# Kernel tuning notes

Hardware: AMD Instinct MI355X
Metric: run time of the kernel (lower is better)

The kernel has to match this reference:

```python
import jax, jax.numpy as jnp
import numpy as np

IN_DIM = 512
HID = 256
SAMPLE = 8
TAU = 0.5
LAMBDA = 1.0
NUM_MLP = 3


def l2norm(x, axis=-1, eps=1e-12):
    n = jnp.sqrt(jnp.sum(x * x, axis=axis, keepdims=True))
    return x / jnp.maximum(n, eps)


def graphconv(adj, x, W, b):
    # GraphConv: aggregate then linear transform
    return adj @ (x @ W) + b


def mlp(x, Ws, bs):
    h = x
    for i in range(len(Ws) - 1):
        h = jax.nn.relu(h @ Ws[i] + bs[i])
    return h @ Ws[-1] + bs[-1]


def setup_inputs() -> dict:
    key = jax.random.key(0)
    ks = jax.random.split(key, 24)
    N = 16384
    # sparse-ish row-normalized adjacency surrogate (dense storage)
    a1 = jax.random.uniform(ks[0], (N, N), jnp.float32)
    a1 = (a1 > 0.999).astype(jnp.float32)
    adj1 = a1 / jnp.maximum(a1.sum(1, keepdims=True), 1.0)
    a2 = jax.random.uniform(ks[1], (N, N), jnp.float32)
    a2 = (a2 > 0.999).astype(jnp.float32)
    adj2 = a2 / jnp.maximum(a2.sum(1, keepdims=True), 1.0)
    x1 = jax.random.normal(ks[2], (N, IN_DIM), jnp.float32)
    x2 = jax.random.normal(ks[3], (N, IN_DIM), jnp.float32)
    neighbor_idx = jax.random.randint(ks[4], (N, SAMPLE), 0, N)
    neg_idx = jax.random.randint(ks[5], (N, SAMPLE), 0, N)

    def lin(k, fi, fo):
        k1, k2 = jax.random.split(k)
        s = 1.0 / np.sqrt(fi)
        return (jax.random.uniform(k1, (fi, fo), jnp.float32, -s, s),
                jax.random.uniform(k2, (fo,), jnp.float32, -s, s))

    W1, b1 = lin(ks[6], IN_DIM, HID)
    W2, b2 = lin(ks[7], HID, HID)
    tW1, tb1 = lin(ks[8], IN_DIM, HID)
    tW2, tb2 = lin(ks[9], HID, HID)
    projW, projB, semW, semB = [], [], [], []
    for i in range(NUM_MLP):
        w, b = lin(ks[10 + i], HID, HID)
        projW.append(w); projB.append(b)
        w, b = lin(ks[14 + i], HID, HID)
        semW.append(w); semB.append(b)
    return dict(adj1=adj1, adj2=adj2, x1=x1, x2=x2,
                neighbor_idx=neighbor_idx, neg_idx=neg_idx,
                W1=W1, b1=b1, W2=W2, b2=b2,
                tW1=tW1, tb1=tb1, tW2=tW2, tb2=tb2,
                projW0=projW[0], projB0=projB[0], projW1=projW[1], projB1=projB[1], projW2=projW[2], projB2=projB[2],
                semW0=semW[0], semB0=semB[0], semW1=semW[1], semB1=semB[1], semW2=semW[2], semB2=semB[2])


def contrastive_loss(projected_emd, v_emd, samp_u, samp_neg_v):
    # projected_emd, v_emd: [N,1,D]; samp_u, samp_neg_v: [N,S,D]
    pos = jnp.exp(jnp.einsum('nod,nsd->ns', projected_emd, samp_u) / TAU)  # [N,S]
    neg_sum = jnp.sum(jnp.exp(jnp.einsum('nod,nsd->ns', v_emd, samp_neg_v) / TAU), axis=1)  # [N]
    neg_score = jnp.sum(jnp.log(pos + neg_sum[:, None]), axis=1)  # [N]
    pos_score = jnp.sum(jnp.log(pos), axis=1)
    total = jnp.sum(LAMBDA * neg_score - pos_score)
    return total / samp_u.shape[0] / samp_u.shape[1]


def semi_loss(z1, z2):
    z1n = l2norm(z1); z2n = l2norm(z2)
    refl = jnp.exp((z1n @ z1n.T) / TAU)      # [N,N]
    between = jnp.exp((z1n @ z2n.T) / TAU)   # [N,N]
    return -jnp.log(jnp.diagonal(between) / (refl.sum(1) + between.sum(1) - jnp.diagonal(refl)))


def reference(adj1, adj2, x1, x2, neighbor_idx, neg_idx,
              W1, b1, W2, b2, tW1, tb1, tW2, tb2,
              projW0, projB0, projW1, projB1, projW2, projB2,
              semW0, semB0, semW1, semB1, semW2, semB2):
    pW = [projW0, projW1, projW2]; pB = [projB0, projB1, projB2]
    sW = [semW0, semW1, semW2]; sB = [semB0, semB1, semB2]
    h1 = graphconv(adj1, x1, W1, b1)
    h2 = graphconv(adj1, x2, W1, b1)
    h3 = graphconv(adj2, graphconv(adj2, x1, W1, b1), W2, b2)  # v_emd
    u_emd = l2norm(graphconv(adj2, graphconv(adj2, x1, tW1, tb1), tW2, tb2))
    projected = l2norm(mlp(h3, pW, pB))
    h1_proj = l2norm(mlp(h1, sW, sB))
    h2_proj = l2norm(mlp(h2, sW, sB))

    v_norm = l2norm(h3)
    samp_u = u_emd[neighbor_idx]          # [N,S,D]
    samp_neg_v = v_norm[neg_idx]          # [N,S,D]
    gacl = contrastive_loss(projected[:, None, :], v_norm[:, None, :], samp_u, samp_neg_v)

    l1 = semi_loss(h1_proj, h2_proj)
    l2 = semi_loss(h2_proj, h1_proj)
    sem = jnp.mean((l1 + l2) * 0.5)

    total = gacl + 0.6 * sem
    return total, gacl, sem, h3
```

## Files before the change

### kernel.cpp

```cpp
#include <hip/hip_runtime.h>
#include <hip/hip_bf16.h>

#define NN   16384
#define IND  512
#define HID  256
#define SAMP 8
#define CAP  64

typedef __bf16 bf16;
typedef __bf16 bf16x4 __attribute__((ext_vector_type(4)));
typedef __bf16 bf16x8 __attribute__((ext_vector_type(8)));
typedef float  f32x4  __attribute__((ext_vector_type(4)));

#define LOG2E_2 2.8853900817779268f

#define GLOAD_LDS16(gptr, lptr) \
  __builtin_amdgcn_global_load_lds((const __attribute__((address_space(1))) void*)(gptr), \
                                   (__attribute__((address_space(3))) void*)(lptr), 16, 0, 0)

__global__ void cvt_x(const float* __restrict__ a, bf16* __restrict__ oa,
                      const float* __restrict__ b, bf16* __restrict__ ob) {
  const float* src = blockIdx.y ? b : a;
  bf16* dst = blockIdx.y ? ob : oa;
  int stride = gridDim.x * blockDim.x;
  for (int i = blockIdx.x * blockDim.x + threadIdx.x; i < (NN * IND) / 4; i += stride) {
    float4 v = ((const float4*)src)[i];
    bf16x4 o = {(bf16)v.x, (bf16)v.y, (bf16)v.z, (bf16)v.w};
    *(bf16x4*)(dst + (size_t)i * 4) = o;
  }
}

struct WtArgs {
  const float* src[10];
  bf16* dst[10];
  int K[10];
};

__global__ void cvt_weights(WtArgs a) {
  int w = blockIdx.y;
  int K = a.K[w];
  int total = K * HID;
  const float* s = a.src[w];
  bf16* d = a.dst[w];
  for (int i = blockIdx.x * blockDim.x + threadIdx.x; i < total; i += gridDim.x * blockDim.x) {
    int k = i >> 8, n = i & 255;
    d[n * K + k] = (bf16)s[i];
  }
}

__global__ void scan_adj(const float* __restrict__ adjA, const float* __restrict__ adjB,
                         int* __restrict__ colsA, int* __restrict__ cntA,
                         int* __restrict__ colsB, int* __restrict__ cntB) {
  const float* adj = blockIdx.y ? adjB : adjA;
  int* cols = blockIdx.y ? colsB : colsA;
  int* cnt = blockIdx.y ? cntB : cntA;
  int r = blockIdx.x;
  __shared__ int c;
  if (threadIdx.x == 0) c = 0;
  __syncthreads();
  const float4* row = (const float4*)(adj + (size_t)r * NN);
  int* rc = cols + (size_t)r * CAP;
  #pragma unroll 4
  for (int i = threadIdx.x; i < NN / 4; i += 256) {
    float4 v = row[i];
    if (v.x != 0.f || v.y != 0.f || v.z != 0.f || v.w != 0.f) {
      if (v.x != 0.f) { int p = atomicAdd(&c, 1); if (p < CAP) rc[p] = 4 * i; }
      if (v.y != 0.f) { int p = atomicAdd(&c, 1); if (p < CAP) rc[p] = 4 * i + 1; }
      if (v.z != 0.f) { int p = atomicAdd(&c, 1); if (p < CAP) rc[p] = 4 * i + 2; }
      if (v.w != 0.f) { int p = atomicAdd(&c, 1); if (p < CAP) rc[p] = 4 * i + 3; }
    }
  }
  __syncthreads();
  if (threadIdx.x == 0) cnt[r] = (c < CAP) ? c : CAP;
}

struct SpmmB {
  const int* cols[4]; const int* cnt[4]; const bf16* X[4]; const float* bias[4];
  float* outF[4];
  bf16* outB[4];
  float* outNF[4];
};
__global__ void spmm_b(SpmmB s) {
  int j = blockIdx.y;
  int wid = threadIdx.x >> 6, lane = threadIdx.x & 63;
  int r = blockIdx.x * 4 + wid;
  int c = s.cnt[j][r];
  float val = 1.0f / (float)(c > 0 ? c : 1);
  const int* rc = s.cols[j] + (size_t)r * CAP;
  const bf16* X = s.X[j];
  float ax = 0.f, ay = 0.f, az = 0.f, aw = 0.f;
  for (int t = 0; t < c; ++t) {
    int col = rc[t];
    bf16x4 v = *(const bf16x4*)(X + (size_t)col * HID + lane * 4);
    ax += (float)v[0]; ay += (float)v[1]; az += (float)v[2]; aw += (float)v[3];
  }
  float4 b4 = ((const float4*)s.bias[j])[lane];
  ax = ax * val + b4.x; ay = ay * val + b4.y; az = az * val + b4.z; aw = aw * val + b4.w;
  if (s.outF[j]) {
    float* o = s.outF[j] + (size_t)r * HID + lane * 4;
    o[0] = ax; o[1] = ay; o[2] = az; o[3] = aw;
  }
  if (s.outB[j]) {
    bf16x4 ob = {(bf16)ax, (bf16)ay, (bf16)az, (bf16)aw};
    *(bf16x4*)(s.outB[j] + (size_t)r * HID + lane * 4) = ob;
  }
  if (s.outNF[j]) {
    float ss = ax * ax + ay * ay + az * az + aw * aw;
    #pragma unroll
    for (int off = 1; off < 64; off <<= 1) ss += __shfl_xor(ss, off);
    float inv = 1.0f / fmaxf(sqrtf(ss), 1e-12f);
    float4 o = {ax * inv, ay * inv, az * inv, aw * inv};
    ((float4*)(s.outNF[j] + (size_t)r * HID))[lane] = o;
  }
}

struct GemmB {
  const bf16* A[3]; const bf16* Bt[3]; const float* bias[3];
  float* Cf[3]; bf16* Cb[3];
};
__global__ __launch_bounds__(256) void gemm_b(GemmB g, int K, int relu) {
  __shared__ bf16 As[128][64];
  __shared__ bf16 Bs[128][64];
  int j = blockIdx.z;
  const bf16* A = g.A[j];
  const bf16* Bt = g.Bt[j];
  int m0 = blockIdx.x * 128, n0 = blockIdx.y * 128;
  int tid = threadIdx.x, wid = tid >> 6, lane = tid & 63;
  int wm = wid >> 1, wn = wid & 1, q = lane >> 4, li = lane & 15;
  int r8 = lane >> 3, cc8 = lane & 7;
  int csw = cc8 ^ r8;
  f32x4 acc[4][4] = {};
  for (int k0 = 0; k0 < K; k0 += 64) {
    if (k0) __syncthreads();
    const bf16* gA = A + (size_t)(m0 + wid * 32 + r8) * K + k0 + csw * 8;
    const bf16* gB = Bt + (size_t)(n0 + wid * 32 + r8) * K + k0 + csw * 8;
    #pragma unroll
    for (int jj = 0; jj < 4; ++jj) {
      GLOAD_LDS16(gA + (size_t)jj * 8 * K, &As[wid * 32 + jj * 8][0]);
      GLOAD_LDS16(gB + (size_t)jj * 8 * K, &Bs[wid * 32 + jj * 8][0]);
    }
    __syncthreads();
    #pragma unroll
    for (int kk = 0; kk < 64; kk += 32) {
      int ca = (((q + (kk >> 3)) ^ (li & 7)) << 3);
      bf16x8 af[4], bfr[4];
      #pragma unroll
      for (int im = 0; im < 4; ++im) af[im] = *(const bf16x8*)(&As[wm * 64 + im * 16 + li][ca]);
      #pragma unroll
      for (int in = 0; in < 4; ++in) bfr[in] = *(const bf16x8*)(&Bs[wn * 64 + in * 16 + li][ca]);
      #pragma unroll
      for (int im = 0; im < 4; ++im)
        #pragma unroll
        for (int in = 0; in < 4; ++in)
          acc[im][in] = __builtin_amdgcn_mfma_f32_16x16x32_bf16(af[im], bfr[in], acc[im][in], 0, 0, 0);
    }
  }
  float* Cf = g.Cf[j];
  bf16* Cb = g.Cb[j];
  const float* bias = g.bias[j];
  #pragma unroll
  for (int im = 0; im < 4; ++im) {
    int grow0 = m0 + wm * 64 + im * 16 + q * 4;
    #pragma unroll
    for (int in = 0; in < 4; ++in) {
      int gcol = n0 + wn * 64 + in * 16 + li;
      float bv = bias ? bias[gcol] : 0.f;
      #pragma unroll
      for (int reg = 0; reg < 4; ++reg) {
        float v = acc[im][in][reg] + bv;
        if (relu) v = fmaxf(v, 0.f);
        size_t idx = (size_t)(grow0 + reg) * HID + gcol;
        if (Cf) Cf[idx] = v;
        if (Cb) Cb[idx] = (bf16)v;
      }
    }
  }
}

__global__ __launch_bounds__(256, 1) void flash_sem5(
    const bf16* __restrict__ P, const bf16* __restrict__ Q,
    float* __restrict__ Ra, float* __restrict__ Rb,
    float* __restrict__ Cr, float* __restrict__ Cc) {
  __shared__ bf16 As[2][128 * 256];
  int z = blockIdx.z;
  const bf16 *X, *Y;
  float* out;
  if (z == 0)      { X = P; Y = P; out = Ra; }
  else if (z == 1) { X = Q; Y = Q; out = Rb; }
  else if (z == 2) { X = P; Y = Q; out = Cc; }
  else             { X = Q; Y = P; out = Cr; }
  int tid = threadIdx.x, wid = tid >> 6, lane = tid & 63;
  int q = lane >> 4, li = lane & 15;
  int cbase = blockIdx.x * 512 + wid * 128;
  bf16x8 bfrag[8][8];
  #pragma unroll
  for (int in = 0; in < 8; ++in) {
    const bf16* Yr = Y + (size_t)(cbase + in * 16 + li) * HID + q * 8;
    #pragma unroll
    for (int kk = 0; kk < 8; ++kk)
      bfrag[in][kk] = *(const bf16x8*)(Yr + kk * 32);
  }
  float cs[8] = {};
  int i0 = blockIdx.y * (NN / 2);
  int l5 = lane >> 5, cp = lane & 31;
  auto stage = [&](int chunk, int b) {
    const bf16* src = X + (size_t)(i0 + chunk * 128) * HID;
    #pragma unroll
    for (int n = 0; n < 16; ++n) {
      int idx = wid * 16 + n;
      int r = idx * 2 + l5;
      int csrc = cp ^ (r & 31);
      GLOAD_LDS16(src + (size_t)r * HID + csrc * 8, &As[b][idx * 512]);
    }
  };
  stage(0, 0);
  __syncthreads();
  for (int c = 0; c < 64; ++c) {
    int b = c & 1;
    if (c + 1 < 64) stage(c + 1, b ^ 1);
    const bf16* buf = &As[b][0];
    #pragma unroll
    for (int ii = 0; ii < 8; ++ii) {
      bf16x8 af[8];
      #pragma unroll
      for (int kk = 0; kk < 8; ++kk) {
        int r = ii * 16 + li;
        int c16 = (kk * 4 + q) ^ (r & 31);
        af[kk] = *(const bf16x8*)(buf + r * 256 + c16 * 8);
      }
      f32x4 acc[8] = {};
      #pragma unroll
      for (int kk = 0; kk < 8; ++kk)
        #pragma unroll
        for (int in = 0; in < 8; ++in)
          acc[in] = __builtin_amdgcn_mfma_f32_16x16x32_bf16(af[kk], bfrag[in][kk], acc[in], 0, 0, 0);
      #pragma unroll
      for (int in = 0; in < 8; ++in)
        #pragma unroll
        for (int reg = 0; reg < 4; ++reg)
          cs[in] += exp2f(acc[in][reg] * LOG2E_2);
    }
    __syncthreads();
  }
  #pragma unroll
  for (int in = 0; in < 8; ++in) {
    float v = cs[in];
    v += __shfl_xor(v, 16);
    v += __shfl_xor(v, 32);
    if (q == 0) atomicAdd(&out[cbase + in * 16 + li], v);
  }
}

struct NormB { const float* X[3]; float* outF[3]; bf16* outB[3]; };
__global__ void l2norm_b(NormB n) {
  int j = blockIdx.y;
  int wid = threadIdx.x >> 6, lane = threadIdx.x & 63;
  int r = blockIdx.x * 4 + wid;
  float4 a = ((const float4*)(n.X[j] + (size_t)r * HID))[lane];
  float s = a.x * a.x + a.y * a.y + a.z * a.z + a.w * a.w;
  #pragma unroll
  for (int off = 1; off < 64; off <<= 1) s += __shfl_xor(s, off);
  float inv = 1.0f / fmaxf(sqrtf(s), 1e-12f);
  a.x *= inv; a.y *= inv; a.z *= inv; a.w *= inv;
  if (n.outF[j]) ((float4*)(n.outF[j] + (size_t)r * HID))[lane] = a;
  if (n.outB[j]) {
    bf16x4 b = {(bf16)a.x, (bf16)a.y, (bf16)a.z, (bf16)a.w};
    *(bf16x4*)(n.outB[j] + (size_t)r * HID + lane * 4) = b;
  }
}

__global__ void tail_k(const float* __restrict__ proj, const float* __restrict__ vn,
                       const float* __restrict__ ue, const int* __restrict__ nbr,
                       const int* __restrict__ neg,
                       const float* __restrict__ P, const float* __restrict__ Q2,
                       const float* __restrict__ Ra, const float* __restrict__ Rb,
                       const float* __restrict__ Cr, const float* __restrict__ Cc,
                       float* __restrict__ sums) {
  int wid = threadIdx.x >> 6, lane = threadIdx.x & 63;
  int n = blockIdx.x * 4 + wid;
  if (blockIdx.y == 0) {
    float4 p = ((const float4*)(proj + (size_t)n * HID))[lane];
    float4 v = ((const float4*)(vn + (size_t)n * HID))[lane];
    float du[SAMP], dn[SAMP];
    for (int s = 0; s < SAMP; ++s) {
      int iu = nbr[n * SAMP + s];
      float4 u = ((const float4*)(ue + (size_t)iu * HID))[lane];
      float d = p.x * u.x + p.y * u.y + p.z * u.z + p.w * u.w;
      #pragma unroll
      for (int off = 1; off < 64; off <<= 1) d += __shfl_xor(d, off);
      du[s] = d;
      int iv = neg[n * SAMP + s];
      float4 w = ((const float4*)(vn + (size_t)iv * HID))[lane];
      float d2 = v.x * w.x + v.y * w.y + v.z * w.z + v.w * w.w;
      #pragma unroll
      for (int off = 1; off < 64; off <<= 1) d2 += __shfl_xor(d2, off);
      dn[s] = d2;
    }
    float negsum = 0.f;
    for (int s = 0; s < SAMP; ++s) negsum += expf(2.f * dn[s]);
    float ns = 0.f, ps = 0.f;
    for (int s = 0; s < SAMP; ++s) {
      float pl = 2.f * du[s];
      ns += logf(expf(pl) + negsum);
      ps += pl;
    }
    if (lane == 0) atomicAdd(&sums[0], ns - ps);
  } else {
    float4 a = ((const float4*)(P + (size_t)n * HID))[lane];
    float4 b = ((const float4*)(Q2 + (size_t)n * HID))[lane];
    float d = a.x * b.x + a.y * b.y + a.z * b.z + a.w * b.w;
    #pragma unroll
    for (int off = 1; off < 64; off <<= 1) d += __shfl_xor(d, off);
    float db = expf(2.f * d);
    float e2 = expf(2.f);
    float l1 = -logf(db / (Ra[n] + Cr[n] - e2));
    float l2 = -logf(db / (Rb[n] + Cc[n] - e2));
    if (lane == 0) atomicAdd(&sums[1], 0.5f * (l1 + l2));
  }
}

__global__ void final_k(const float* __restrict__ sums, float* __restrict__ out) {
  float gacl = sums[0] / (float)(NN * SAMP);
  float sem = sums[1] / (float)NN;
  out[0] = gacl + 0.6f * sem;
  out[1] = gacl;
  out[2] = sem;
}

extern "C" void kernel_launch(void* const* d_in, const int* in_sizes, int n_in,
                              void* d_out, int out_size, void* d_ws, size_t ws_size,
                              hipStream_t stream) {
  (void)in_sizes; (void)n_in; (void)out_size; (void)ws_size;
  const float* adj1 = (const float*)d_in[0];
  const float* adj2 = (const float*)d_in[1];
  const float* x1 = (const float*)d_in[2];
  const float* x2 = (const float*)d_in[3];
  const int* nbr = (const int*)d_in[4];
  const int* neg = (const int*)d_in[5];
  const float* W1 = (const float*)d_in[6];
  const float* b1 = (const float*)d_in[7];
  const float* W2 = (const float*)d_in[8];
  const float* b2 = (const float*)d_in[9];
  const float* tW1 = (const float*)d_in[10];
  const float* tb1 = (const float*)d_in[11];
  const float* tW2 = (const float*)d_in[12];
  const float* tb2 = (const float*)d_in[13];
  const float* pB[3] = {(const float*)d_in[15], (const float*)d_in[17], (const float*)d_in[19]};
  const float* sB[3] = {(const float*)d_in[21], (const float*)d_in[23], (const float*)d_in[25]};

  char* w = (char*)d_ws;
  auto alloc = [&](size_t bytes) -> char* {
    char* p = w;
    w += (bytes + 255) & ~(size_t)255;
    return p;
  };
  float* Ra = (float*)alloc((size_t)NN * 4);
  float* Rb = (float*)alloc((size_t)NN * 4);
  float* Cr = (float*)alloc((size_t)NN * 4);
  float* Cc = (float*)alloc((size_t)NN * 4);
  float* sums = (float*)alloc(256);
  size_t accBytes = (size_t)(w - (char*)d_ws);

  int* c1cols = (int*)alloc((size_t)NN * CAP * 4);
  int* c1cnt = (int*)alloc((size_t)NN * 4);
  int* c2cols = (int*)alloc((size_t)NN * CAP * 4);
  int* c2cnt = (int*)alloc((size_t)NN * 4);
  bf16* x1b = (bf16*)alloc((size_t)NN * IND * 2);
  bf16* x2b = (bf16*)alloc((size_t)NN * IND * 2);
  bf16* W1t = (bf16*)alloc((size_t)IND * HID * 2);
  bf16* tW1t = (bf16*)alloc((size_t)IND * HID * 2);
  bf16* W2t = (bf16*)alloc((size_t)HID * HID * 2);
  bf16* tW2t = (bf16*)alloc((size_t)HID * HID * 2);
  bf16* pWt[3], *sWt[3];
  for (int i = 0; i < 3; ++i) pWt[i] = (bf16*)alloc((size_t)HID * HID * 2);
  for (int i = 0; i < 3; ++i) sWt[i] = (bf16*)alloc((size_t)HID * HID * 2);
  const size_t BB = (size_t)NN * HID * 2;
  bf16* xw1b = (bf16*)alloc(BB);
  bf16* xw2b = (bf16*)alloc(BB);
  bf16* xt1b = (bf16*)alloc(BB);
  bf16* gwb = (bf16*)alloc(BB);
  bf16* utwb = (bf16*)alloc(BB);
  bf16* h1b = (bf16*)alloc(BB);
  bf16* h2b = (bf16*)alloc(BB);
  bf16* gb_ = (bf16*)alloc(BB);
  bf16* h3b = (bf16*)alloc(BB);
  bf16* utb = (bf16*)alloc(BB);
  bf16* mA = (bf16*)alloc(BB);
  bf16* mB = (bf16*)alloc(BB);
  bf16* mB1 = (bf16*)alloc(BB);
  bf16* mB2 = (bf16*)alloc(BB);
  bf16* Pb = (bf16*)alloc(BB);
  bf16* Qb = (bf16*)alloc(BB);
  const size_t FB = (size_t)NN * HID * 4;
  float* u_emd = (float*)alloc(FB);
  float* v_norm = (float*)alloc(FB);
  float* projected = (float*)alloc(FB);
  float* h1p = (float*)alloc(FB);
  float* h2p = (float*)alloc(FB);
  float* mlp_out = (float*)alloc(FB);
  float* s3a = (float*)alloc(FB);
  float* s3b = (float*)alloc(FB);

  hipMemsetAsync(d_ws, 0, accBytes, stream);

  WtArgs wa;
  const float* wsrc[10] = {W1, tW1, W2, tW2,
                           (const float*)d_in[14], (const float*)d_in[16], (const float*)d_in[18],
                           (const float*)d_in[20], (const float*)d_in[22], (const float*)d_in[24]};
  bf16* wdst[10] = {W1t, tW1t, W2t, tW2t, pWt[0], pWt[1], pWt[2], sWt[0], sWt[1], sWt[2]};
  int wk[10] = {IND, IND, HID, HID, HID, HID, HID, HID, HID, HID};
  for (int i = 0; i < 10; ++i) { wa.src[i] = wsrc[i]; wa.dst[i] = wdst[i]; wa.K[i] = wk[i]; }
  cvt_weights<<<dim3(512, 10), 256, 0, stream>>>(wa);
  cvt_x<<<dim3(2048, 2), 256, 0, stream>>>(x1, x1b, x2, x2b);
  scan_adj<<<dim3(NN, 2), 256, 0, stream>>>(adj1, adj2, c1cols, c1cnt, c2cols, c2cnt);

  {
    GemmB g = {};
    g.A[0] = x1b; g.Bt[0] = W1t; g.Cb[0] = xw1b;
    g.A[1] = x2b; g.Bt[1] = W1t; g.Cb[1] = xw2b;
    g.A[2] = x1b; g.Bt[2] = tW1t; g.Cb[2] = xt1b;
    gemm_b<<<dim3(128, 2, 3), 256, 0, stream>>>(g, IND, 0);
  }
  {
    SpmmB s = {};
    s.cols[0] = c1cols; s.cnt[0] = c1cnt; s.X[0] = xw1b; s.bias[0] = b1; s.outB[0] = h1b;
    s.cols[1] = c1cols; s.cnt[1] = c1cnt; s.X[1] = xw2b; s.bias[1] = b1; s.outB[1] = h2b;
    s.cols[2] = c2cols; s.cnt[2] = c2cnt; s.X[2] = xw1b; s.bias[2] = b1; s.outB[2] = gb_;
    s.cols[3] = c2cols; s.cnt[3] = c2cnt; s.X[3] = xt1b; s.bias[3] = tb1; s.outB[3] = utb;
    spmm_b<<<dim3(NN / 4, 4), 256, 0, stream>>>(s);
  }
  {
    GemmB g = {};
    g.A[0] = gb_; g.Bt[0] = W2t; g.Cb[0] = gwb;
    g.A[1] = utb; g.Bt[1] = tW2t; g.Cb[1] = utwb;
    gemm_b<<<dim3(128, 2, 2), 256, 0, stream>>>(g, HID, 0);
  }
  float* h3out = ((float*)d_out) + 3;
  {
    SpmmB s = {};
    s.cols[0] = c2cols; s.cnt[0] = c2cnt; s.X[0] = gwb; s.bias[0] = b2;
    s.outF[0] = h3out; s.outB[0] = h3b; s.outNF[0] = v_norm;
    s.cols[1] = c2cols; s.cnt[1] = c2cnt; s.X[1] = utwb; s.bias[1] = tb2;
    s.outNF[1] = u_emd;
    spmm_b<<<dim3(NN / 4, 2), 256, 0, stream>>>(s);
  }
  {
    GemmB g = {};
    g.A[0] = h3b; g.Bt[0] = pWt[0]; g.bias[0] = pB[0]; g.Cb[0] = mA;
    g.A[1] = h1b; g.Bt[1] = sWt[0]; g.bias[1] = sB[0]; g.Cb[1] = gb_;
    g.A[2] = h2b; g.Bt[2] = sWt[0]; g.bias[2] = sB[0]; g.Cb[2] = utb;
    gemm_b<<<dim3(128, 2, 3), 256, 0, stream>>>(g, HID, 1);
  }
  {
    GemmB g = {};
    g.A[0] = mA; g.Bt[0] = pWt[1]; g.bias[0] = pB[1]; g.Cb[0] = mB;
    g.A[1] = gb_; g.Bt[1] = sWt[1]; g.bias[1] = sB[1]; g.Cb[1] = mB1;
    g.A[2] = utb; g.Bt[2] = sWt[1]; g.bias[2] = sB[1]; g.Cb[2] = mB2;
    gemm_b<<<dim3(128, 2, 3), 256, 0, stream>>>(g, HID, 1);
  }
  {
    GemmB g = {};
    g.A[0] = mB; g.Bt[0] = pWt[2]; g.bias[0] = pB[2]; g.Cf[0] = mlp_out;
    g.A[1] = mB1; g.Bt[1] = sWt[2]; g.bias[1] = sB[2]; g.Cf[1] = s3a;
    g.A[2] = mB2; g.Bt[2] = sWt[2]; g.bias[2] = sB[2]; g.Cf[2] = s3b;
    gemm_b<<<dim3(128, 2, 3), 256, 0, stream>>>(g, HID, 0);
  }
  {
    NormB nb2 = {};
    nb2.X[0] = mlp_out; nb2.outF[0] = projected;
    nb2.X[1] = s3a; nb2.outF[1] = h1p; nb2.outB[1] = Pb;
    nb2.X[2] = s3b; nb2.outF[2] = h2p; nb2.outB[2] = Qb;
    l2norm_b<<<dim3(NN / 4, 3), 256, 0, stream>>>(nb2);
  }

  flash_sem5<<<dim3(32, 2, 4), 256, 0, stream>>>(Pb, Qb, Ra, Rb, Cr, Cc);
  tail_k<<<dim3(NN / 4, 2), 256, 0, stream>>>(projected, v_norm, u_emd, nbr, neg,
                                              h1p, h2p, Ra, Rb, Cr, Cc, sums);
  final_k<<<1, 1, 0, stream>>>(sums, (float*)d_out);
}
```

Measured before the change: 3.723 ms.

## Exploit symmetry of self-similarity in fused semantic-loss exp-sum kernel

```diff
diff --git a/kernel.cpp b/kernel.cpp
--- a/kernel.cpp
+++ b/kernel.cpp
@@ -177,77 +177,129 @@
   }
 }
 
-__global__ __launch_bounds__(256, 1) void flash_sem5(
+__global__ __launch_bounds__(512, 2) void flash_sem6(
     const bf16* __restrict__ P, const bf16* __restrict__ Q,
     float* __restrict__ Ra, float* __restrict__ Rb,
     float* __restrict__ Cr, float* __restrict__ Cc) {
-  __shared__ bf16 As[2][128 * 256];
+  __shared__ bf16 Xs[2][64 * 256];
+  __shared__ bf16 Zs[2][64 * 256];
   int z = blockIdx.z;
-  const bf16 *X, *Y;
-  float* out;
-  if (z == 0)      { X = P; Y = P; out = Ra; }
-  else if (z == 1) { X = Q; Y = Q; out = Rb; }
-  else if (z == 2) { X = P; Y = Q; out = Cc; }
-  else             { X = Q; Y = P; out = Cr; }
+  const bf16* Y  = z ? Q : P;
+  const bf16* Xg = z ? Q : P;
+  const bf16* Zg = z ? P : Q;
+  float* outS = z ? Rb : Ra;
+  float* outC = z ? Cc : Cr;
   int tid = threadIdx.x, wid = tid >> 6, lane = tid & 63;
   int q = lane >> 4, li = lane & 15;
-  int cbase = blockIdx.x * 512 + wid * 128;
-  bf16x8 bfrag[8][8];
+  int cbase = blockIdx.x * 512;
+  int cw = cbase + wid * 64;
+  int i0 = blockIdx.y * 4096;
+  bf16x8 bfrag[4][8];
   #pragma unroll
-  for (int in = 0; in < 8; ++in) {
-    const bf16* Yr = Y + (size_t)(cbase + in * 16 + li) * HID + q * 8;
+  for (int in = 0; in < 4; ++in) {
+    const bf16* Yr = Y + (size_t)(cw + in * 16 + li) * HID + q * 8;
     #pragma unroll
     for (int kk = 0; kk < 8; ++kk)
       bfrag[in][kk] = *(const bf16x8*)(Yr + kk * 32);
   }
-  float cs[8] = {};
-  int i0 = blockIdx.y * (NN / 2);
-  int l5 = lane >> 5, cp = lane & 31;
-  auto stage = [&](int chunk, int b) {
-    const bf16* src = X + (size_t)(i0 + chunk * 128) * HID;
-    #pragma unroll
-    for (int n = 0; n < 16; ++n) {
-      int idx = wid * 16 + n;
-      int r = idx * 2 + l5;
-      int csrc = cp ^ (r & 31);
-      GLOAD_LDS16(src + (size_t)r * HID + csrc * 8, &As[b][idx * 512]);
+  float csS[4] = {}, csC[4] = {};
+  int l5 = lane >> 5, c16 = lane & 31;
+  auto stage = [&](const bf16* g, bf16* ldsbase, int c) {
+    const bf16* src = g + (size_t)(i0 + c * 64) * HID;
+    #pragma unroll
+    for (int n = 0; n < 4; ++n) {
+      int rl = wid * 8 + n * 2;
+      int r = rl + l5;
+      int cs_ = c16 ^ (r & 31);
+      GLOAD_LDS16(src + (size_t)r * HID + cs_ * 8, ldsbase + rl * 256);
     }
   };
-  stage(0, 0);
+  auto needX = [&](int c) { return (i0 + c * 64) < cbase + 512; };
+  stage(Zg, &Xs[0][0] + 0, 0);
+  __syncthreads();
+  stage(Zg, &Zs[0][0], 0);
+  if (needX(0)) stage(Xg, &Xs[0][0], 0);
   __syncthreads();
   for (int c = 0; c < 64; ++c) {
     int b = c & 1;
-    if (c + 1 < 64) stage(c + 1, b ^ 1);
-    const bf16* buf = &As[b][0];
-    #pragma unroll
-    for (int ii = 0; ii < 8; ++ii) {
+    if (c + 1 < 64) {
+      stage(Zg, &Zs[b ^ 1][0], c + 1);
+      if (needX(c + 1)) stage(Xg, &Xs[b ^ 1][0], c + 1);
+    }
+    #pragma unroll
+    for (int ii = 0; ii < 4; ++ii) {
       bf16x8 af[8];
       #pragma unroll
       for (int kk = 0; kk < 8; ++kk) {
-        int r = ii * 16 + li;
-        int c16 = (kk * 4 + q) ^ (r & 31);
-        af[kk] = *(const bf16x8*)(buf + r * 256 + c16 * 8);
+        int row = ii * 16 + li;
+        af[kk] = *(const bf16x8*)(&Zs[b][row * 256 + (((kk * 4 + q) ^ (row & 31)) << 3)]);
       }
-      f32x4 acc[8] = {};
-      #pragma unroll
-      for (int kk = 0; kk < 8; ++kk)
+      #pragma unroll
+      for (int in = 0; in < 4; ++in) {
+        f32x4 acc = {};
         #pragma unroll
-        for (int in = 0; in < 8; ++in)
-          acc[in] = __builtin_amdgcn_mfma_f32_16x16x32_bf16(af[kk], bfrag[in][kk], acc[in], 0, 0, 0);
-      #pragma unroll
-      for (int in = 0; in < 8; ++in)
+        for (int kk = 0; kk < 8; ++kk)
+          acc = __builtin_amdgcn_mfma_f32_16x16x32_bf16(af[kk], bfrag[in][kk], acc, 0, 0, 0);
         #pragma unroll
         for (int reg = 0; reg < 4; ++reg)
-          cs[in] += exp2f(acc[in][reg] * LOG2E_2);
+          csC[in] += exp2f(acc[reg] * LOG2E_2);
+      }
+    }
+    int rchunk = i0 + c * 64;
+    if (rchunk < cbase + 512) {
+      #pragma unroll
+      for (int ii = 0; ii < 4; ++ii) {
+        int rt = rchunk + ii * 16;
+        if (rt >= cw + 64) continue;
+        bf16x8 af[8];
+        #pragma unroll
+        for (int kk = 0; kk < 8; ++kk) {
+          int row = ii * 16 + li;
+          af[kk] = *(const bf16x8*)(&Xs[b][row * 256 + (((kk * 4 + q) ^ (row & 31)) << 3)]);
+        }
+        #pragma unroll
+        for (int in = 0; in < 4; ++in) {
+          int ct = cw + in * 16;
+          if (rt >= ct + 16) continue;
+          f32x4 acc = {};
+          #pragma unroll
+          for (int kk = 0; kk < 8; ++kk)
+            acc = __builtin_amdgcn_mfma_f32_16x16x32_bf16(af[kk], bfrag[in][kk], acc, 0, 0, 0);
+          if (rt + 16 <= ct) {
+            #pragma unroll
+            for (int reg = 0; reg < 4; ++reg) {
+              float e = exp2f(acc[reg] * LOG2E_2);
+              csS[in] += e;
+              float rs = e;
+              rs += __shfl_xor(rs, 1); rs += __shfl_xor(rs, 2);
+              rs += __shfl_xor(rs, 4); rs += __shfl_xor(rs, 8);
+              if (li == 0) atomicAdd(&outS[rt + q * 4 + reg], rs);
+            }
+          } else {
+            #pragma unroll
+            for (int reg = 0; reg < 4; ++reg) {
+              float e = exp2f(acc[reg] * LOG2E_2);
+              int row = q * 4 + reg;
+              csS[in] += (row <= li) ? e : 0.f;
+              float rs = (row < li) ? e : 0.f;
+              rs += __shfl_xor(rs, 1); rs += __shfl_xor(rs, 2);
+              rs += __shfl_xor(rs, 4); rs += __shfl_xor(rs, 8);
+              if (li == 0) atomicAdd(&outS[rt + row], rs);
+            }
+          }
+        }
+      }
     }
     __syncthreads();
   }
   #pragma unroll
-  for (int in = 0; in < 8; ++in) {
-    float v = cs[in];
-    v += __shfl_xor(v, 16);
-    v += __shfl_xor(v, 32);
-    if (q == 0) atomicAdd(&out[cbase + in * 16 + li], v);
+  for (int in = 0; in < 4; ++in) {
+    float v = csC[in];
+    v += __shfl_xor(v, 16); v += __shfl_xor(v, 32);
+    if (q == 0) atomicAdd(&outC[cw + in * 16 + li], v);
+    float u = csS[in];
+    u += __shfl_xor(u, 16); u += __shfl_xor(u, 32);
+    if (q == 0) atomicAdd(&outS[cw + in * 16 + li], u);
   }
 }
 
@@ -473,7 +525,7 @@
     l2norm_b<<<dim3(NN / 4, 3), 256, 0, stream>>>(nb2);
   }
 
-  flash_sem5<<<dim3(32, 2, 4), 256, 0, stream>>>(Pb, Qb, Ra, Rb, Cr, Cc);
+  flash_sem6<<<dim3(32, 4, 2), 512, 0, stream>>>(Pb, Qb, Ra, Rb, Cr, Cc);
   tail_k<<<dim3(NN / 4, 2), 256, 0, stream>>>(projected, v_norm, u_emd, nbr, neg,
                                               h1p, h2p, Ra, Rb, Cr, Cc, sums);
   final_k<<<1, 1, 0, stream>>>(sums, (float*)d_out);
```

New measurement: 5.267 ms. 1.41x slower.
